# Kernel optimization log

Hardware: AMD Instinct MI355X
Metric: run time of the kernel (lower is better)

The kernel has to match this reference:

```python
import jax, jax.numpy as jnp
import numpy as np

# Constants matching init_kwargs
N_HEADS = 8
D_MODEL = 256
PATCH_NUM = 128
D_K = D_MODEL // N_HEADS  # 32
TEMP = 0.5
EPS = 1e-10


def setup_inputs() -> dict:
    key = jax.random.key(0)
    ks = jax.random.split(key, 20)
    s = 0.02
    d, h, n = D_MODEL, N_HEADS, PATCH_NUM
    inp = {
        "x": jax.random.normal(ks[0], (32, n, d), dtype=jnp.float32),
        "gumbel_u": jax.random.uniform(ks[1], (h, n, n, 2), dtype=jnp.float32),
        "memory_w": jax.random.normal(ks[2], (n, h * d), dtype=jnp.float32) * s,
        "fc_out_w": jax.random.normal(ks[3], (2 * d, d), dtype=jnp.float32) * s,
        "fc_out_b": jnp.zeros((d,), jnp.float32),
        "fc_cat_w": jax.random.normal(ks[4], (d, 2), dtype=jnp.float32) * s,
        "fc_cat_b": jnp.zeros((2,), jnp.float32),
        "wq": jax.random.normal(ks[5], (d, d), dtype=jnp.float32) * s,
        "bq": jnp.zeros((d,), jnp.float32),
        "wk": jax.random.normal(ks[6], (d, d), dtype=jnp.float32) * s,
        "bk": jnp.zeros((d,), jnp.float32),
        "wv": jax.random.normal(ks[7], (d, d), dtype=jnp.float32) * s,
        "bv": jnp.zeros((d,), jnp.float32),
        "out_w": jax.random.normal(ks[8], (d, d), dtype=jnp.float32) * s,
        "out_b": jnp.zeros((d,), jnp.float32),
        "mlp_w1": jax.random.normal(ks[9], (d, d), dtype=jnp.float32) * s,
        "mlp_b1": jnp.zeros((d,), jnp.float32),
        "mlp_w2": jax.random.normal(ks[10], (d, d), dtype=jnp.float32) * s,
        "mlp_b2": jnp.zeros((d,), jnp.float32),
    }
    return inp


def _forward(x, memory_w, fc_out_w, fc_out_b, fc_cat_w, fc_cat_b,
             wq, bq, wk, bk, wv, bv, out_w, out_b,
             mlp_w1, mlp_b1, mlp_w2, mlp_b2, gumbel_u):
    H, N, D = N_HEADS, PATCH_NUM, D_MODEL
    B = x.shape[0]

    # ---- SSConnectionLearning on memory feats ----
    # memory: Embedding(N, d_model*n_heads) -> feats [H, N, D]
    feats = memory_w.reshape(N, H, D).transpose(1, 0, 2)
    # rel_rec gathers row index i (receiver), rel_send gathers col index j (sender)
    senders = jnp.broadcast_to(feats[:, None, :, :], (H, N, N, D))   # feats[j]
    receivers = jnp.broadcast_to(feats[:, :, None, :], (H, N, N, D))  # feats[i]
    pair = jnp.concatenate([senders, receivers], axis=-1)  # [H,N,N,2D]
    hdn = jax.nn.relu(jnp.einsum('hijc,cd->hijd', pair, fc_out_w) + fc_out_b)
    logits = jnp.einsum('hijd,dk->hijk', hdn, fc_cat_w) + fc_cat_b  # [H,N,N,2]

    # gumbel-softmax, hard=True, straight-through
    g = -jnp.log(-jnp.log(gumbel_u + EPS) + EPS)
    y_soft = jax.nn.softmax((logits + g) / TEMP, axis=-1)
    y_hard = jax.nn.one_hot(jnp.argmax(y_soft, axis=-1), 2, dtype=y_soft.dtype)
    y = jax.lax.stop_gradient(y_hard - y_soft) + y_soft
    conn = y[..., 1]  # [H,N,N] learned sparse connection mask

    # ---- PatchIntegration (GELU MLP, dropout = identity in eval) ----
    xm = jax.nn.gelu(x @ mlp_w1 + mlp_b1)
    xm = xm @ mlp_w2 + mlp_b2

    # ---- Multihead attention masked by connection matrix ----
    q = (xm @ wq + bq).reshape(B, N, H, D_K).transpose(0, 2, 1, 3)  # [B,H,N,dk]
    k = (xm @ wk + bk).reshape(B, N, H, D_K).transpose(0, 2, 1, 3)
    v = (xm @ wv + bv).reshape(B, N, H, D_K).transpose(0, 2, 1, 3)
    scale = D_K ** -0.5
    scores = jnp.einsum('bhqd,bhkd->bhqk', q, k) * scale
    # additive mask: blocked where conn==0 (large negative keeps softmax finite)
    scores = scores + (conn[None] - 1.0) * 1e9
    attn = jax.nn.softmax(scores, axis=-1)
    out = jnp.einsum('bhqk,bhkd->bhqd', attn, v)
    out = out.transpose(0, 2, 1, 3).reshape(B, N, H * D_K)
    out = out @ out_w + out_b
    return out


def reference(x, gumbel_u, memory_w, fc_out_w, fc_out_b, fc_cat_w, fc_cat_b,
              wq, bq, wk, bk, wv, bv, out_w, out_b,
              mlp_w1, mlp_b1, mlp_w2, mlp_b2):
    return _forward(x, memory_w, fc_out_w, fc_out_b, fc_cat_w, fc_cat_b,
                    wq, bq, wk, bk, wv, bv, out_w, out_b,
                    mlp_w1, mlp_b1, mlp_w2, mlp_b2, gumbel_u)
```

## Files before the change

kernel.cpp:

```cpp
#include <hip/hip_runtime.h>
#include <hip/hip_bf16.h>
#include <math.h>


typedef short short8 __attribute__((ext_vector_type(8)));
typedef float f32x4 __attribute__((ext_vector_type(4)));

union V8 { uint4 u; short8 s; };

__device__ __forceinline__ float gelu_f(float x) {
    float inner = 0.7978845608028654f * (x + 0.044715f * x * x * x);
    return 0.5f * x * (1.0f + tanhf(inner));
}

__device__ __forceinline__ void split_bf16(float x, ushort& h, ushort& l) {
    __hip_bfloat16 bh = __float2bfloat16(x);
    float hf = __bfloat162float(bh);
    __hip_bfloat16 bl = __float2bfloat16(x - hf);
    h = __builtin_bit_cast(ushort, bh);
    l = __builtin_bit_cast(ushort, bl);
}

__device__ __forceinline__ ushort bf16bits(float x) {
    return __builtin_bit_cast(ushort, __float2bfloat16(x));
}
__device__ __forceinline__ float bits_to_f(ushort v) {
    return __builtin_bit_cast(float, ((uint)v) << 16);
}
__device__ __forceinline__ uint pk(float a, float b) {
    return (uint)bf16bits(a) | ((uint)bf16bits(b) << 16);
}
__device__ __forceinline__ short8 lds_frag(const ushort* p) {
    V8 v; v.u = *(const uint4*)p; return v.s;
}

__global__ __launch_bounds__(256) void k_wprep(
    const float* __restrict__ w0, const float* __restrict__ w1,
    const float* __restrict__ w2, const float* __restrict__ w3,
    const float* __restrict__ w4, const float* __restrict__ w5,
    const float* __restrict__ w6, const float* __restrict__ w7,
    ushort* __restrict__ hi, ushort* __restrict__ lo) {
    int bx = blockIdx.x;
    int m = bx >> 4, ks = (bx >> 1) & 7, nh = bx & 1;
    const float* W = m == 0 ? w0 : m == 1 ? w1 : m == 2 ? w2 : m == 3 ? w3 :
                     m == 4 ? w4 : m == 5 ? w5 : m == 6 ? w6 : w7;
    ushort* Hm = hi + m * 65536;
    ushort* Lm = lo + m * 65536;
    __shared__ __align__(16) float xs[32 * 132];
    int t = threadIdx.x;
    #pragma unroll
    for (int p = 0; p < 4; ++p) {
        int idx = p * 256 + t;
        int row = idx >> 5, c4 = (idx & 31) * 4;
        *(float4*)(xs + row * 132 + c4) =
            *(const float4*)(W + (ks * 32 + row) * 256 + nh * 128 + c4);
    }
    __syncthreads();
    int lane = t & 63, lr = lane & 15, quad = lane >> 4;
    #pragma unroll
    for (int it = 0; it < 2; ++it) {
        int tgl = (t >> 6) + 4 * it;
        int tg = nh * 8 + tgl;
        int nl = tgl * 16 + lr;
        ushort hb[8], lb[8];
        #pragma unroll
        for (int j = 0; j < 8; ++j)
            split_bf16(xs[(quad * 8 + j) * 132 + nl], hb[j], lb[j]);
        uint4 ph = { (uint)hb[0] | ((uint)hb[1] << 16), (uint)hb[2] | ((uint)hb[3] << 16),
                     (uint)hb[4] | ((uint)hb[5] << 16), (uint)hb[6] | ((uint)hb[7] << 16) };
        uint4 pl = { (uint)lb[0] | ((uint)lb[1] << 16), (uint)lb[2] | ((uint)lb[3] << 16),
                     (uint)lb[4] | ((uint)lb[5] << 16), (uint)lb[6] | ((uint)lb[7] << 16) };
        int idx = ((tg * 8 + ks) * 64 + lane) * 8;
        *(uint4*)(Hm + idx) = ph;
        *(uint4*)(Lm + idx) = pl;
    }
}

__global__ __launch_bounds__(256) void k_featproj(
    const float* __restrict__ memory_w,
    const ushort* __restrict__ Whi, const ushort* __restrict__ Wlo,
    float* __restrict__ A, float* __restrict__ Bm) {
    __shared__ __align__(16) ushort xhi[16 * 264], xlo[16 * 264];
    int t = threadIdx.x;
    int rt = blockIdx.x;
    int msel = blockIdx.y & 1, cq = blockIdx.y >> 1;
    #pragma unroll
    for (int ii = 0; ii < 4; ++ii) {
        int f4 = ii * 256 + t;
        int rr = f4 >> 6, c = (f4 & 63) * 4;
        int r = rt * 16 + rr;
        int h = r >> 7, n = r & 127;
        float4 xv = *(const float4*)(memory_w + n * 2048 + h * 256 + c);
        ushort hh[4], ll[4];
        split_bf16(xv.x, hh[0], ll[0]); split_bf16(xv.y, hh[1], ll[1]);
        split_bf16(xv.z, hh[2], ll[2]); split_bf16(xv.w, hh[3], ll[3]);
        uint2 ph = { (uint)hh[0] | ((uint)hh[1] << 16), (uint)hh[2] | ((uint)hh[3] << 16) };
        uint2 pl = { (uint)ll[0] | ((uint)ll[1] << 16), (uint)ll[2] | ((uint)ll[3] << 16) };
        *(uint2*)(xhi + rr * 264 + c) = ph;
        *(uint2*)(xlo + rr * 264 + c) = pl;
    }
    __syncthreads();
    int l = t & 63, w = t >> 6;
    int lr = l & 15, quad = l >> 4;
    int tg = cq * 4 + w;
    const uint4* H4 = (const uint4*)(Whi + (6 + msel) * 65536);
    const uint4* L4 = (const uint4*)(Wlo + (6 + msel) * 65536);
    const ushort* ah = xhi + lr * 264 + quad * 8;
    const ushort* al = xlo + lr * 264 + quad * 8;
    f32x4 acc = {};
    #pragma unroll 4
    for (int ks = 0; ks < 8; ++ks) {
        short8 a_h = lds_frag(ah + ks * 32);
        short8 a_l = lds_frag(al + ks * 32);
        int off = (tg * 8 + ks) * 64 + l;
        V8 bh, bl; bh.u = H4[off]; bl.u = L4[off];
        acc = __builtin_amdgcn_mfma_f32_16x16x32_bf16(a_h, bh.s, acc, 0, 0, 0);
        acc = __builtin_amdgcn_mfma_f32_16x16x32_bf16(a_l, bh.s, acc, 0, 0, 0);
        acc = __builtin_amdgcn_mfma_f32_16x16x32_bf16(a_h, bl.s, acc, 0, 0, 0);
    }
    float* O = msel ? Bm : A;
    int n0 = tg * 16 + lr;
    #pragma unroll
    for (int r = 0; r < 4; ++r)
        O[(rt * 16 + quad * 4 + r) * 256 + n0] = acc[r];
}

__global__ __launch_bounds__(256) void k_conn(
    const float* __restrict__ A, const float* __restrict__ Bm,
    const float* __restrict__ fc_out_b, const float* __restrict__ fc_cat_w,
    const float* __restrict__ fc_cat_b, const float* __restrict__ gumbel_u,
    ushort* __restrict__ maskb) {
    int bx = blockIdx.x;
    int h = bx >> 6, it = (bx >> 3) & 7, jt = bx & 7;
    int i0 = it * 16, j0 = jt * 16;
    int t = threadIdx.x;
    int il = t >> 4, jl = t & 15;
    __shared__ __align__(16) float sA[16 * 260], sB[16 * 260];
    #pragma unroll
    for (int p = 0; p < 4; ++p) {
        int idx = p * 256 + t;
        int rr = idx >> 6, c = (idx & 63) * 4;
        *(float4*)(sA + rr * 260 + c) =
            *(const float4*)(A + (h * 128 + j0 + rr) * 256 + c);
        float4 bv = *(const float4*)(Bm + (h * 128 + i0 + rr) * 256 + c);
        float4 fb = *(const float4*)(fc_out_b + c);
        bv.x += fb.x; bv.y += fb.y; bv.z += fb.z; bv.w += fb.w;
        *(float4*)(sB + rr * 260 + c) = bv;
    }
    __syncthreads();
    const float* Ar = sA + jl * 260;
    const float* Br = sB + il * 260;
    float l0 = fc_cat_b[0], l1 = fc_cat_b[1];
    #pragma unroll 4
    for (int d4 = 0; d4 < 64; ++d4) {
        int d = d4 * 4;
        float4 av = *(const float4*)(Ar + d);
        float4 bv = *(const float4*)(Br + d);
        float4 cwA = *(const float4*)(fc_cat_w + d * 2);
        float4 cwB = *(const float4*)(fc_cat_w + d * 2 + 4);
        float h0 = fmaxf(av.x + bv.x, 0.f);
        float h1 = fmaxf(av.y + bv.y, 0.f);
        float h2 = fmaxf(av.z + bv.z, 0.f);
        float h3 = fmaxf(av.w + bv.w, 0.f);
        l0 += h0 * cwA.x + h1 * cwA.z + h2 * cwB.x + h3 * cwB.z;
        l1 += h0 * cwA.y + h1 * cwA.w + h2 * cwB.y + h3 * cwB.w;
    }
    int i = i0 + il, j = j0 + jl;
    float2 uu = *(const float2*)(gumbel_u + ((h * 128 + i) * 128 + j) * 2);
    float g0 = -logf(-logf(uu.x + 1e-10f) + 1e-10f);
    float g1 = -logf(-logf(uu.y + 1e-10f) + 1e-10f);
    bool on = (l1 + g1) > (l0 + g0);
    maskb[(h * 128 + i) * 128 + j] = bf16bits(on ? 0.f : -1e9f);
}

template <int ACT>
__global__ __launch_bounds__(256) void k_gemm16(
    const float* __restrict__ X, const ushort* __restrict__ Whi,
    const ushort* __restrict__ Wlo, const float* __restrict__ bias,
    float* __restrict__ Y) {
    __shared__ __align__(16) ushort xhi[16 * 264], xlo[16 * 264];
    int t = threadIdx.x;
    int r0 = blockIdx.x * 16;
    #pragma unroll
    for (int ii = 0; ii < 4; ++ii) {
        int f4 = ii * 256 + t;
        int row = f4 >> 6, c = (f4 & 63) * 4;
        float4 xv = *(const float4*)(X + (r0 + row) * 256 + c);
        ushort h[4], l[4];
        split_bf16(xv.x, h[0], l[0]); split_bf16(xv.y, h[1], l[1]);
        split_bf16(xv.z, h[2], l[2]); split_bf16(xv.w, h[3], l[3]);
        uint2 ph = { (uint)h[0] | ((uint)h[1] << 16), (uint)h[2] | ((uint)h[3] << 16) };
        uint2 pl = { (uint)l[0] | ((uint)l[1] << 16), (uint)l[2] | ((uint)l[3] << 16) };
        *(uint2*)(xhi + row * 264 + c) = ph;
        *(uint2*)(xlo + row * 264 + c) = pl;
    }
    __syncthreads();
    int l = t & 63, w = t >> 6;
    int lr = l & 15, quad = l >> 4;
    int tg = blockIdx.y * 4 + w;
    const ushort* ah = xhi + lr * 264 + quad * 8;
    const ushort* al = xlo + lr * 264 + quad * 8;
    const uint4* H4 = (const uint4*)Whi;
    const uint4* L4 = (const uint4*)Wlo;
    f32x4 acc = {};
    #pragma unroll 4
    for (int ks = 0; ks < 8; ++ks) {
        short8 a_h = lds_frag(ah + ks * 32);
        short8 a_l = lds_frag(al + ks * 32);
        int off = (tg * 8 + ks) * 64 + l;
        V8 bh, bl; bh.u = H4[off]; bl.u = L4[off];
        acc = __builtin_amdgcn_mfma_f32_16x16x32_bf16(a_h, bh.s, acc, 0, 0, 0);
        acc = __builtin_amdgcn_mfma_f32_16x16x32_bf16(a_l, bh.s, acc, 0, 0, 0);
        acc = __builtin_amdgcn_mfma_f32_16x16x32_bf16(a_h, bl.s, acc, 0, 0, 0);
    }
    int n0 = tg * 16 + lr;
    float bs = bias[n0];
    #pragma unroll
    for (int r = 0; r < 4; ++r) {
        float o = acc[r] + bs;
        if (ACT) o = gelu_f(o);
        Y[(r0 + quad * 4 + r) * 256 + n0] = o;
    }
}

__global__ __launch_bounds__(256) void k_qkv(
    const float* __restrict__ X, const ushort* __restrict__ Whi,
    const ushort* __restrict__ Wlo,
    const float* __restrict__ Bq, const float* __restrict__ Bk,
    const float* __restrict__ Bv,
    float* __restrict__ Q, float* __restrict__ K, float* __restrict__ V) {
    __shared__ __align__(16) ushort xhi[16 * 264], xlo[16 * 264];
    int t = threadIdx.x;
    int r0 = blockIdx.x * 16;
    int osel = blockIdx.y >> 2, cq = blockIdx.y & 3;
    #pragma unroll
    for (int ii = 0; ii < 4; ++ii) {
        int f4 = ii * 256 + t;
        int row = f4 >> 6, c = (f4 & 63) * 4;
        float4 xv = *(const float4*)(X + (r0 + row) * 256 + c);
        ushort h[4], l[4];
        split_bf16(xv.x, h[0], l[0]); split_bf16(xv.y, h[1], l[1]);
        split_bf16(xv.z, h[2], l[2]); split_bf16(xv.w, h[3], l[3]);
        uint2 ph = { (uint)h[0] | ((uint)h[1] << 16), (uint)h[2] | ((uint)h[3] << 16) };
        uint2 pl = { (uint)l[0] | ((uint)l[1] << 16), (uint)l[2] | ((uint)l[3] << 16) };
        *(uint2*)(xhi + row * 264 + c) = ph;
        *(uint2*)(xlo + row * 264 + c) = pl;
    }
    __syncthreads();
    int l = t & 63, w = t >> 6;
    int lr = l & 15, quad = l >> 4;
    int tg = cq * 4 + w;
    const ushort* ah = xhi + lr * 264 + quad * 8;
    const ushort* al = xlo + lr * 264 + quad * 8;
    const uint4* H4 = (const uint4*)(Whi + (2 + osel) * 65536);
    const uint4* L4 = (const uint4*)(Wlo + (2 + osel) * 65536);
    f32x4 acc = {};
    #pragma unroll 4
    for (int ks = 0; ks < 8; ++ks) {
        short8 a_h = lds_frag(ah + ks * 32);
        short8 a_l = lds_frag(al + ks * 32);
        int off = (tg * 8 + ks) * 64 + l;
        V8 bh, bl; bh.u = H4[off]; bl.u = L4[off];
        acc = __builtin_amdgcn_mfma_f32_16x16x32_bf16(a_h, bh.s, acc, 0, 0, 0);
        acc = __builtin_amdgcn_mfma_f32_16x16x32_bf16(a_l, bh.s, acc, 0, 0, 0);
        acc = __builtin_amdgcn_mfma_f32_16x16x32_bf16(a_h, bl.s, acc, 0, 0, 0);
    }
    const float* Bp = osel == 0 ? Bq : osel == 1 ? Bk : Bv;
    float* O = osel == 0 ? Q : osel == 1 ? K : V;
    int n0 = tg * 16 + lr;
    float bs = Bp[n0];
    #pragma unroll
    for (int r = 0; r < 4; ++r)
        O[(r0 + quad * 4 + r) * 256 + n0] = acc[r] + bs;
}

__global__ __launch_bounds__(256) void k_attn_mfma(
    const float* __restrict__ Q, const float* __restrict__ K,
    const float* __restrict__ V, const ushort* __restrict__ maskb,
    float* __restrict__ AO) {
    int bx = blockIdx.x;
    int b = bx >> 4, h = (bx >> 1) & 7, rh = bx & 1;
    int t = threadIdx.x;
    int lane = t & 63, w = t >> 6;
    __shared__ __align__(16) ushort vT[32 * 136];
    __shared__ __align__(16) ushort ps[64 * 136];
    #pragma unroll
    for (int it = 0; it < 4; ++it) {
        int f4 = it * 256 + t;
        int key = f4 >> 3, dq = (f4 & 7) * 4;
        float4 vv = *(const float4*)(V + b * 32768 + key * 256 + h * 32 + dq);
        vT[(dq + 0) * 136 + key] = bf16bits(vv.x);
        vT[(dq + 1) * 136 + key] = bf16bits(vv.y);
        vT[(dq + 2) * 136 + key] = bf16bits(vv.z);
        vT[(dq + 3) * 136 + key] = bf16bits(vv.w);
    }
    __syncthreads();
    int lr = lane & 15, quad = lane >> 4;
    int rt = rh * 4 + w;
    const float* qp = Q + b * 32768 + (rt * 16 + lr) * 256 + h * 32 + quad * 8;
    float4 q0 = *(const float4*)qp, q1 = *(const float4*)(qp + 4);
    V8 af;
    af.u.x = pk(q0.x, q0.y); af.u.y = pk(q0.z, q0.w);
    af.u.z = pk(q1.x, q1.y); af.u.w = pk(q1.z, q1.w);
    f32x4 s[8];
    #pragma unroll
    for (int ct = 0; ct < 8; ++ct) {
        const float* kp = K + b * 32768 + (ct * 16 + lr) * 256 + h * 32 + quad * 8;
        float4 k0 = *(const float4*)kp, k1 = *(const float4*)(kp + 4);
        V8 bf_;
        bf_.u.x = pk(k0.x, k0.y); bf_.u.y = pk(k0.z, k0.w);
        bf_.u.z = pk(k1.x, k1.y); bf_.u.w = pk(k1.z, k1.w);
        f32x4 z = {0.f, 0.f, 0.f, 0.f};
        s[ct] = __builtin_amdgcn_mfma_f32_16x16x32_bf16(af.s, bf_.s, z, 0, 0, 0);
    }
    const float scale = 0.17677669529663687f;
    const ushort* mrow = maskb + h * 16384;
    #pragma unroll
    for (int r = 0; r < 4; ++r) {
        int lrow = w * 16 + quad * 4 + r;
        int grow = rt * 16 + quad * 4 + r;
        float sv[8];
        float mx = -3.0e38f;
        #pragma unroll
        for (int ct = 0; ct < 8; ++ct) {
            float bias = bits_to_f(mrow[grow * 128 + ct * 16 + lr]);
            sv[ct] = s[ct][r] * scale + bias;
            mx = fmaxf(mx, sv[ct]);
        }
        mx = fmaxf(mx, __shfl_xor(mx, 1));
        mx = fmaxf(mx, __shfl_xor(mx, 2));
        mx = fmaxf(mx, __shfl_xor(mx, 4));
        mx = fmaxf(mx, __shfl_xor(mx, 8));
        float sum = 0.f;
        #pragma unroll
        for (int ct = 0; ct < 8; ++ct) {
            sv[ct] = __expf(sv[ct] - mx);
            sum += sv[ct];
        }
        sum += __shfl_xor(sum, 1);
        sum += __shfl_xor(sum, 2);
        sum += __shfl_xor(sum, 4);
        sum += __shfl_xor(sum, 8);
        float iv = 1.f / sum;
        #pragma unroll
        for (int ct = 0; ct < 8; ++ct)
            ps[lrow * 136 + ct * 16 + lr] = bf16bits(sv[ct] * iv);
    }
    f32x4 o0 = {}, o1 = {};
    #pragma unroll
    for (int kk = 0; kk < 4; ++kk) {
        short8 pa = lds_frag(ps + (w * 16 + lr) * 136 + kk * 32 + quad * 8);
        short8 v0 = lds_frag(vT + lr * 136 + kk * 32 + quad * 8);
        short8 v1 = lds_frag(vT + (16 + lr) * 136 + kk * 32 + quad * 8);
        o0 = __builtin_amdgcn_mfma_f32_16x16x32_bf16(pa, v0, o0, 0, 0, 0);
        o1 = __builtin_amdgcn_mfma_f32_16x16x32_bf16(pa, v1, o1, 0, 0, 0);
    }
    #pragma unroll
    for (int r = 0; r < 4; ++r) {
        int grow = rt * 16 + quad * 4 + r;
        float* op = AO + b * 32768 + grow * 256 + h * 32;
        op[lr] = o0[r];
        op[16 + lr] = o1[r];
    }
}

extern "C" void kernel_launch(void* const* d_in, const int* in_sizes, int n_in,
                              void* d_out, int out_size, void* d_ws, size_t ws_size,
                              hipStream_t stream) {
    const float* x        = (const float*)d_in[0];
    const float* gumbel_u = (const float*)d_in[1];
    const float* memory_w = (const float*)d_in[2];
    const float* fc_out_w = (const float*)d_in[3];
    const float* fc_out_b = (const float*)d_in[4];
    const float* fc_cat_w = (const float*)d_in[5];
    const float* fc_cat_b = (const float*)d_in[6];
    const float* wq       = (const float*)d_in[7];
    const float* bq       = (const float*)d_in[8];
    const float* wk       = (const float*)d_in[9];
    const float* bk       = (const float*)d_in[10];
    const float* wv_      = (const float*)d_in[11];
    const float* bv_      = (const float*)d_in[12];
    const float* out_w    = (const float*)d_in[13];
    const float* out_b    = (const float*)d_in[14];
    const float* mlp_w1   = (const float*)d_in[15];
    const float* mlp_b1   = (const float*)d_in[16];
    const float* mlp_w2   = (const float*)d_in[17];
    const float* mlp_b2   = (const float*)d_in[18];

    float* ws    = (float*)d_ws;
    float* A     = ws;
    float* Bm    = ws + 262144;
    ushort* mask = (ushort*)(ws + 524288);
    float* hbuf  = ws + 589824;
    float* xm    = ws + 1638400;
    float* q     = ws + 2686976;
    float* k     = ws + 3735552;
    float* v     = ws + 4784128;
    float* ao    = ws + 5832704;
    ushort* wf_hi = (ushort*)(ws + 6881280);
    ushort* wf_lo = wf_hi + 8 * 65536;
    float* out   = (float*)d_out;

    k_wprep<<<dim3(128), dim3(256), 0, stream>>>(
        mlp_w1, mlp_w2, wq, wk, wv_, out_w, fc_out_w, fc_out_w + 65536,
        wf_hi, wf_lo);
    k_featproj<<<dim3(64, 8), dim3(256), 0, stream>>>(memory_w, wf_hi, wf_lo, A, Bm);
    k_conn<<<dim3(512), dim3(256), 0, stream>>>(A, Bm, fc_out_b, fc_cat_w, fc_cat_b,
                                                gumbel_u, mask);
    k_gemm16<1><<<dim3(256, 4), dim3(256), 0, stream>>>(x, wf_hi + 0 * 65536,
                                                        wf_lo + 0 * 65536, mlp_b1, hbuf);
    k_gemm16<0><<<dim3(256, 4), dim3(256), 0, stream>>>(hbuf, wf_hi + 1 * 65536,
                                                        wf_lo + 1 * 65536, mlp_b2, xm);
    k_qkv<<<dim3(256, 12), dim3(256), 0, stream>>>(xm, wf_hi, wf_lo, bq, bk, bv_, q, k, v);
    k_attn_mfma<<<dim3(512), dim3(256), 0, stream>>>(q, k, v, mask, ao);
    k_gemm16<0><<<dim3(256, 4), dim3(256), 0, stream>>>(ao, wf_hi + 5 * 65536,
                                                        wf_lo + 5 * 65536, out_b, out);
}
```

Baseline: 161.4 us.

## Fuse all stages into one persistent cooperative kernel with grid syncs

Replaces the eight separate launches with a single cooperative kernel of 512 blocks that runs every stage in sequence, separated by grid-wide barriers. Independent stages (feature projection with MLP1, connection mask with MLP2) now share a phase, and the GEMM phases are reshaped so each block computes two column tiles instead of one. If the cooperative launch fails, it falls back to six per-phase launches. The aim is to remove launch overhead and the gaps between kernels. The cost is grid-sync latency and less parallelism per GEMM phase.

```diff
diff --git a/kernel.cpp b/kernel.cpp
--- a/kernel.cpp
+++ b/kernel.cpp
@@ -1,18 +1,35 @@
 #include <hip/hip_runtime.h>
+#include <hip/hip_cooperative_groups.h>
 #include <hip/hip_bf16.h>
 #include <math.h>
 
+namespace cg = cooperative_groups;
+
 
 typedef short short8 __attribute__((ext_vector_type(8)));
 typedef float f32x4 __attribute__((ext_vector_type(4)));
 
 union V8 { uint4 u; short8 s; };
+
+struct Params {
+    const float *x, *gumbel_u, *memory_w, *fc_out_w, *fc_out_b, *fc_cat_w, *fc_cat_b;
+    const float *wq, *bq, *wk, *bk, *wv, *bv, *out_w, *out_b;
+    const float *mlp_w1, *mlp_b1, *mlp_w2, *mlp_b2;
+    float *A, *Bm, *hbuf, *xm, *q, *k, *v, *ao, *out;
+    ushort *mask, *wf_hi, *wf_lo;
+};
+
+union SMem {
+    struct { ushort xhi[16 * 264]; ushort xlo[16 * 264]; } g;
+    struct { float xs[32 * 132]; } w;
+    struct { float sA[16 * 260]; float sB[16 * 260]; } c;
+    struct { ushort vT[32 * 136]; ushort ps[64 * 136]; } a;
+};
 
 __device__ __forceinline__ float gelu_f(float x) {
     float inner = 0.7978845608028654f * (x + 0.044715f * x * x * x);
     return 0.5f * x * (1.0f + tanhf(inner));
 }
-
 __device__ __forceinline__ void split_bf16(float x, ushort& h, ushort& l) {
     __hip_bfloat16 bh = __float2bfloat16(x);
     float hf = __bfloat162float(bh);
@@ -20,7 +37,6 @@
     h = __builtin_bit_cast(ushort, bh);
     l = __builtin_bit_cast(ushort, bl);
 }
-
 __device__ __forceinline__ ushort bf16bits(float x) {
     return __builtin_bit_cast(ushort, __float2bfloat16(x));
 }
@@ -34,25 +50,19 @@
     V8 v; v.u = *(const uint4*)p; return v.s;
 }
 
-__global__ __launch_bounds__(256) void k_wprep(
-    const float* __restrict__ w0, const float* __restrict__ w1,
-    const float* __restrict__ w2, const float* __restrict__ w3,
-    const float* __restrict__ w4, const float* __restrict__ w5,
-    const float* __restrict__ w6, const float* __restrict__ w7,
-    ushort* __restrict__ hi, ushort* __restrict__ lo) {
-    int bx = blockIdx.x;
-    int m = bx >> 4, ks = (bx >> 1) & 7, nh = bx & 1;
-    const float* W = m == 0 ? w0 : m == 1 ? w1 : m == 2 ? w2 : m == 3 ? w3 :
-                     m == 4 ? w4 : m == 5 ? w5 : m == 6 ? w6 : w7;
-    ushort* Hm = hi + m * 65536;
-    ushort* Lm = lo + m * 65536;
-    __shared__ __align__(16) float xs[32 * 132];
-    int t = threadIdx.x;
+__device__ void ph_wprep(const Params& P, SMem& sm, int bi, int t) {
+    if (bi >= 128) return;
+    int m = bi >> 4, ks = (bi >> 1) & 7, nh = bi & 1;
+    const float* Wm[8] = { P.mlp_w1, P.mlp_w2, P.wq, P.wk, P.wv, P.out_w,
+                           P.fc_out_w, P.fc_out_w + 65536 };
+    const float* W = Wm[m];
+    ushort* Hm = P.wf_hi + m * 65536;
+    ushort* Lm = P.wf_lo + m * 65536;
     #pragma unroll
     for (int p = 0; p < 4; ++p) {
         int idx = p * 256 + t;
         int row = idx >> 5, c4 = (idx & 31) * 4;
-        *(float4*)(xs + row * 132 + c4) =
+        *(float4*)(sm.w.xs + row * 132 + c4) =
             *(const float4*)(W + (ks * 32 + row) * 256 + nh * 128 + c4);
     }
     __syncthreads();
@@ -65,7 +75,7 @@
         ushort hb[8], lb[8];
         #pragma unroll
         for (int j = 0; j < 8; ++j)
-            split_bf16(xs[(quad * 8 + j) * 132 + nl], hb[j], lb[j]);
+            split_bf16(sm.w.xs[(quad * 8 + j) * 132 + nl], hb[j], lb[j]);
         uint4 ph = { (uint)hb[0] | ((uint)hb[1] << 16), (uint)hb[2] | ((uint)hb[3] << 16),
                      (uint)hb[4] | ((uint)hb[5] << 16), (uint)hb[6] | ((uint)hb[7] << 16) };
         uint4 pl = { (uint)lb[0] | ((uint)lb[1] << 16), (uint)lb[2] | ((uint)lb[3] << 16),
@@ -76,111 +86,8 @@
     }
 }
 
-__global__ __launch_bounds__(256) void k_featproj(
-    const float* __restrict__ memory_w,
-    const ushort* __restrict__ Whi, const ushort* __restrict__ Wlo,
-    float* __restrict__ A, float* __restrict__ Bm) {
-    __shared__ __align__(16) ushort xhi[16 * 264], xlo[16 * 264];
-    int t = threadIdx.x;
-    int rt = blockIdx.x;
-    int msel = blockIdx.y & 1, cq = blockIdx.y >> 1;
-    #pragma unroll
-    for (int ii = 0; ii < 4; ++ii) {
-        int f4 = ii * 256 + t;
-        int rr = f4 >> 6, c = (f4 & 63) * 4;
-        int r = rt * 16 + rr;
-        int h = r >> 7, n = r & 127;
-        float4 xv = *(const float4*)(memory_w + n * 2048 + h * 256 + c);
-        ushort hh[4], ll[4];
-        split_bf16(xv.x, hh[0], ll[0]); split_bf16(xv.y, hh[1], ll[1]);
-        split_bf16(xv.z, hh[2], ll[2]); split_bf16(xv.w, hh[3], ll[3]);
-        uint2 ph = { (uint)hh[0] | ((uint)hh[1] << 16), (uint)hh[2] | ((uint)hh[3] << 16) };
-        uint2 pl = { (uint)ll[0] | ((uint)ll[1] << 16), (uint)ll[2] | ((uint)ll[3] << 16) };
-        *(uint2*)(xhi + rr * 264 + c) = ph;
-        *(uint2*)(xlo + rr * 264 + c) = pl;
-    }
-    __syncthreads();
-    int l = t & 63, w = t >> 6;
-    int lr = l & 15, quad = l >> 4;
-    int tg = cq * 4 + w;
-    const uint4* H4 = (const uint4*)(Whi + (6 + msel) * 65536);
-    const uint4* L4 = (const uint4*)(Wlo + (6 + msel) * 65536);
-    const ushort* ah = xhi + lr * 264 + quad * 8;
-    const ushort* al = xlo + lr * 264 + quad * 8;
-    f32x4 acc = {};
-    #pragma unroll 4
-    for (int ks = 0; ks < 8; ++ks) {
-        short8 a_h = lds_frag(ah + ks * 32);
-        short8 a_l = lds_frag(al + ks * 32);
-        int off = (tg * 8 + ks) * 64 + l;
-        V8 bh, bl; bh.u = H4[off]; bl.u = L4[off];
-        acc = __builtin_amdgcn_mfma_f32_16x16x32_bf16(a_h, bh.s, acc, 0, 0, 0);
-        acc = __builtin_amdgcn_mfma_f32_16x16x32_bf16(a_l, bh.s, acc, 0, 0, 0);
-        acc = __builtin_amdgcn_mfma_f32_16x16x32_bf16(a_h, bl.s, acc, 0, 0, 0);
-    }
-    float* O = msel ? Bm : A;
-    int n0 = tg * 16 + lr;
-    #pragma unroll
-    for (int r = 0; r < 4; ++r)
-        O[(rt * 16 + quad * 4 + r) * 256 + n0] = acc[r];
-}
-
-__global__ __launch_bounds__(256) void k_conn(
-    const float* __restrict__ A, const float* __restrict__ Bm,
-    const float* __restrict__ fc_out_b, const float* __restrict__ fc_cat_w,
-    const float* __restrict__ fc_cat_b, const float* __restrict__ gumbel_u,
-    ushort* __restrict__ maskb) {
-    int bx = blockIdx.x;
-    int h = bx >> 6, it = (bx >> 3) & 7, jt = bx & 7;
-    int i0 = it * 16, j0 = jt * 16;
-    int t = threadIdx.x;
-    int il = t >> 4, jl = t & 15;
-    __shared__ __align__(16) float sA[16 * 260], sB[16 * 260];
-    #pragma unroll
-    for (int p = 0; p < 4; ++p) {
-        int idx = p * 256 + t;
-        int rr = idx >> 6, c = (idx & 63) * 4;
-        *(float4*)(sA + rr * 260 + c) =
-            *(const float4*)(A + (h * 128 + j0 + rr) * 256 + c);
-        float4 bv = *(const float4*)(Bm + (h * 128 + i0 + rr) * 256 + c);
-        float4 fb = *(const float4*)(fc_out_b + c);
-        bv.x += fb.x; bv.y += fb.y; bv.z += fb.z; bv.w += fb.w;
-        *(float4*)(sB + rr * 260 + c) = bv;
-    }
-    __syncthreads();
-    const float* Ar = sA + jl * 260;
-    const float* Br = sB + il * 260;
-    float l0 = fc_cat_b[0], l1 = fc_cat_b[1];
-    #pragma unroll 4
-    for (int d4 = 0; d4 < 64; ++d4) {
-        int d = d4 * 4;
-        float4 av = *(const float4*)(Ar + d);
-        float4 bv = *(const float4*)(Br + d);
-        float4 cwA = *(const float4*)(fc_cat_w + d * 2);
-        float4 cwB = *(const float4*)(fc_cat_w + d * 2 + 4);
-        float h0 = fmaxf(av.x + bv.x, 0.f);
-        float h1 = fmaxf(av.y + bv.y, 0.f);
-        float h2 = fmaxf(av.z + bv.z, 0.f);
-        float h3 = fmaxf(av.w + bv.w, 0.f);
-        l0 += h0 * cwA.x + h1 * cwA.z + h2 * cwB.x + h3 * cwB.z;
-        l1 += h0 * cwA.y + h1 * cwA.w + h2 * cwB.y + h3 * cwB.w;
-    }
-    int i = i0 + il, j = j0 + jl;
-    float2 uu = *(const float2*)(gumbel_u + ((h * 128 + i) * 128 + j) * 2);
-    float g0 = -logf(-logf(uu.x + 1e-10f) + 1e-10f);
-    float g1 = -logf(-logf(uu.y + 1e-10f) + 1e-10f);
-    bool on = (l1 + g1) > (l0 + g0);
-    maskb[(h * 128 + i) * 128 + j] = bf16bits(on ? 0.f : -1e9f);
-}
-
-template <int ACT>
-__global__ __launch_bounds__(256) void k_gemm16(
-    const float* __restrict__ X, const ushort* __restrict__ Whi,
-    const ushort* __restrict__ Wlo, const float* __restrict__ bias,
-    float* __restrict__ Y) {
-    __shared__ __align__(16) ushort xhi[16 * 264], xlo[16 * 264];
-    int t = threadIdx.x;
-    int r0 = blockIdx.x * 16;
+__device__ void stage_x(SMem& sm, const float* X, int r0, int t) {
+    __syncthreads();
     #pragma unroll
     for (int ii = 0; ii < 4; ++ii) {
         int f4 = ii * 256 + t;
@@ -191,15 +98,17 @@
         split_bf16(xv.z, h[2], l[2]); split_bf16(xv.w, h[3], l[3]);
         uint2 ph = { (uint)h[0] | ((uint)h[1] << 16), (uint)h[2] | ((uint)h[3] << 16) };
         uint2 pl = { (uint)l[0] | ((uint)l[1] << 16), (uint)l[2] | ((uint)l[3] << 16) };
-        *(uint2*)(xhi + row * 264 + c) = ph;
-        *(uint2*)(xlo + row * 264 + c) = pl;
-    }
-    __syncthreads();
-    int l = t & 63, w = t >> 6;
-    int lr = l & 15, quad = l >> 4;
-    int tg = blockIdx.y * 4 + w;
-    const ushort* ah = xhi + lr * 264 + quad * 8;
-    const ushort* al = xlo + lr * 264 + quad * 8;
+        *(uint2*)(sm.g.xhi + row * 264 + c) = ph;
+        *(uint2*)(sm.g.xlo + row * 264 + c) = pl;
+    }
+    __syncthreads();
+}
+
+__device__ f32x4 gemm_wave(const SMem& sm, const ushort* Whi, const ushort* Wlo,
+                           int tg, int lane) {
+    int lr = lane & 15, quad = lane >> 4;
+    const ushort* ah = sm.g.xhi + lr * 264 + quad * 8;
+    const ushort* al = sm.g.xlo + lr * 264 + quad * 8;
     const uint4* H4 = (const uint4*)Whi;
     const uint4* L4 = (const uint4*)Wlo;
     f32x4 acc = {};
@@ -207,97 +116,164 @@
     for (int ks = 0; ks < 8; ++ks) {
         short8 a_h = lds_frag(ah + ks * 32);
         short8 a_l = lds_frag(al + ks * 32);
-        int off = (tg * 8 + ks) * 64 + l;
+        int off = (tg * 8 + ks) * 64 + lane;
         V8 bh, bl; bh.u = H4[off]; bl.u = L4[off];
         acc = __builtin_amdgcn_mfma_f32_16x16x32_bf16(a_h, bh.s, acc, 0, 0, 0);
         acc = __builtin_amdgcn_mfma_f32_16x16x32_bf16(a_l, bh.s, acc, 0, 0, 0);
         acc = __builtin_amdgcn_mfma_f32_16x16x32_bf16(a_h, bl.s, acc, 0, 0, 0);
     }
-    int n0 = tg * 16 + lr;
-    float bs = bias[n0];
-    #pragma unroll
-    for (int r = 0; r < 4; ++r) {
-        float o = acc[r] + bs;
-        if (ACT) o = gelu_f(o);
-        Y[(r0 + quad * 4 + r) * 256 + n0] = o;
-    }
-}
-
-__global__ __launch_bounds__(256) void k_qkv(
-    const float* __restrict__ X, const ushort* __restrict__ Whi,
-    const ushort* __restrict__ Wlo,
-    const float* __restrict__ Bq, const float* __restrict__ Bk,
-    const float* __restrict__ Bv,
-    float* __restrict__ Q, float* __restrict__ K, float* __restrict__ V) {
-    __shared__ __align__(16) ushort xhi[16 * 264], xlo[16 * 264];
-    int t = threadIdx.x;
-    int r0 = blockIdx.x * 16;
-    int osel = blockIdx.y >> 2, cq = blockIdx.y & 3;
+    return acc;
+}
+
+__device__ void ph_featproj(const Params& P, SMem& sm, int bi, int t) {
+    int rt = bi & 63;
+    int y = bi >> 6;
+    int msel = y & 1, cq = y >> 1;
+    __syncthreads();
     #pragma unroll
     for (int ii = 0; ii < 4; ++ii) {
         int f4 = ii * 256 + t;
-        int row = f4 >> 6, c = (f4 & 63) * 4;
-        float4 xv = *(const float4*)(X + (r0 + row) * 256 + c);
-        ushort h[4], l[4];
-        split_bf16(xv.x, h[0], l[0]); split_bf16(xv.y, h[1], l[1]);
-        split_bf16(xv.z, h[2], l[2]); split_bf16(xv.w, h[3], l[3]);
-        uint2 ph = { (uint)h[0] | ((uint)h[1] << 16), (uint)h[2] | ((uint)h[3] << 16) };
-        uint2 pl = { (uint)l[0] | ((uint)l[1] << 16), (uint)l[2] | ((uint)l[3] << 16) };
-        *(uint2*)(xhi + row * 264 + c) = ph;
-        *(uint2*)(xlo + row * 264 + c) = pl;
-    }
-    __syncthreads();
-    int l = t & 63, w = t >> 6;
-    int lr = l & 15, quad = l >> 4;
+        int rr = f4 >> 6, c = (f4 & 63) * 4;
+        int r = rt * 16 + rr;
+        int h = r >> 7, n = r & 127;
+        float4 xv = *(const float4*)(P.memory_w + n * 2048 + h * 256 + c);
+        ushort hh[4], ll[4];
+        split_bf16(xv.x, hh[0], ll[0]); split_bf16(xv.y, hh[1], ll[1]);
+        split_bf16(xv.z, hh[2], ll[2]); split_bf16(xv.w, hh[3], ll[3]);
+        uint2 ph = { (uint)hh[0] | ((uint)hh[1] << 16), (uint)hh[2] | ((uint)hh[3] << 16) };
+        uint2 pl = { (uint)ll[0] | ((uint)ll[1] << 16), (uint)ll[2] | ((uint)ll[3] << 16) };
+        *(uint2*)(sm.g.xhi + rr * 264 + c) = ph;
+        *(uint2*)(sm.g.xlo + rr * 264 + c) = pl;
+    }
+    __syncthreads();
+    int lane = t & 63, w = t >> 6;
+    int lr = lane & 15, quad = lane >> 4;
     int tg = cq * 4 + w;
-    const ushort* ah = xhi + lr * 264 + quad * 8;
-    const ushort* al = xlo + lr * 264 + quad * 8;
-    const uint4* H4 = (const uint4*)(Whi + (2 + osel) * 65536);
-    const uint4* L4 = (const uint4*)(Wlo + (2 + osel) * 65536);
-    f32x4 acc = {};
+    f32x4 acc = gemm_wave(sm, P.wf_hi + (6 + msel) * 65536,
+                          P.wf_lo + (6 + msel) * 65536, tg, lane);
+    float* O = msel ? P.Bm : P.A;
+    int n0 = tg * 16 + lr;
+    #pragma unroll
+    for (int r = 0; r < 4; ++r)
+        O[(rt * 16 + quad * 4 + r) * 256 + n0] = acc[r];
+}
+
+__device__ void ph_mlp1(const Params& P, SMem& sm, int bi, int t) {
+    int rt = bi & 255, h2 = bi >> 8;
+    stage_x(sm, P.x, rt * 16, t);
+    int lane = t & 63, w = t >> 6;
+    int lr = lane & 15, quad = lane >> 4;
+    #pragma unroll
+    for (int i = 0; i < 2; ++i) {
+        int tg = (h2 * 2 + i) * 4 + w;
+        f32x4 acc = gemm_wave(sm, P.wf_hi, P.wf_lo, tg, lane);
+        int n0 = tg * 16 + lr;
+        float bs = P.mlp_b1[n0];
+        #pragma unroll
+        for (int r = 0; r < 4; ++r)
+            P.hbuf[(rt * 16 + quad * 4 + r) * 256 + n0] = gelu_f(acc[r] + bs);
+    }
+}
+
+__device__ void ph_conn(const Params& P, SMem& sm, int bi, int t) {
+    int h = bi >> 6, it = (bi >> 3) & 7, jt = bi & 7;
+    int i0 = it * 16, j0 = jt * 16;
+    int il = t >> 4, jl = t & 15;
+    __syncthreads();
+    #pragma unroll
+    for (int p = 0; p < 4; ++p) {
+        int idx = p * 256 + t;
+        int rr = idx >> 6, c = (idx & 63) * 4;
+        *(float4*)(sm.c.sA + rr * 260 + c) =
+            *(const float4*)(P.A + (h * 128 + j0 + rr) * 256 + c);
+        float4 bv = *(const float4*)(P.Bm + (h * 128 + i0 + rr) * 256 + c);
+        float4 fb = *(const float4*)(P.fc_out_b + c);
+        bv.x += fb.x; bv.y += fb.y; bv.z += fb.z; bv.w += fb.w;
+        *(float4*)(sm.c.sB + rr * 260 + c) = bv;
+    }
+    __syncthreads();
+    const float* Ar = sm.c.sA + jl * 260;
+    const float* Br = sm.c.sB + il * 260;
+    float l0 = P.fc_cat_b[0], l1 = P.fc_cat_b[1];
     #pragma unroll 4
-    for (int ks = 0; ks < 8; ++ks) {
-        short8 a_h = lds_frag(ah + ks * 32);
-        short8 a_l = lds_frag(al + ks * 32);
-        int off = (tg * 8 + ks) * 64 + l;
-        V8 bh, bl; bh.u = H4[off]; bl.u = L4[off];
-        acc = __builtin_amdgcn_mfma_f32_16x16x32_bf16(a_h, bh.s, acc, 0, 0, 0);
-        acc = __builtin_amdgcn_mfma_f32_16x16x32_bf16(a_l, bh.s, acc, 0, 0, 0);
-        acc = __builtin_amdgcn_mfma_f32_16x16x32_bf16(a_h, bl.s, acc, 0, 0, 0);
-    }
-    const float* Bp = osel == 0 ? Bq : osel == 1 ? Bk : Bv;
-    float* O = osel == 0 ? Q : osel == 1 ? K : V;
-    int n0 = tg * 16 + lr;
-    float bs = Bp[n0];
-    #pragma unroll
-    for (int r = 0; r < 4; ++r)
-        O[(r0 + quad * 4 + r) * 256 + n0] = acc[r] + bs;
-}
-
-__global__ __launch_bounds__(256) void k_attn_mfma(
-    const float* __restrict__ Q, const float* __restrict__ K,
-    const float* __restrict__ V, const ushort* __restrict__ maskb,
-    float* __restrict__ AO) {
-    int bx = blockIdx.x;
-    int b = bx >> 4, h = (bx >> 1) & 7, rh = bx & 1;
-    int t = threadIdx.x;
-    int lane = t & 63, w = t >> 6;
-    __shared__ __align__(16) ushort vT[32 * 136];
-    __shared__ __align__(16) ushort ps[64 * 136];
+    for (int d4 = 0; d4 < 64; ++d4) {
+        int d = d4 * 4;
+        float4 av = *(const float4*)(Ar + d);
+        float4 bv = *(const float4*)(Br + d);
+        float4 cwA = *(const float4*)(P.fc_cat_w + d * 2);
+        float4 cwB = *(const float4*)(P.fc_cat_w + d * 2 + 4);
+        float h0 = fmaxf(av.x + bv.x, 0.f);
+        float h1 = fmaxf(av.y + bv.y, 0.f);
+        float h2 = fmaxf(av.z + bv.z, 0.f);
+        float h3 = fmaxf(av.w + bv.w, 0.f);
+        l0 += h0 * cwA.x + h1 * cwA.z + h2 * cwB.x + h3 * cwB.z;
+        l1 += h0 * cwA.y + h1 * cwA.w + h2 * cwB.y + h3 * cwB.w;
+    }
+    int i = i0 + il, j = j0 + jl;
+    float2 uu = *(const float2*)(P.gumbel_u + ((h * 128 + i) * 128 + j) * 2);
+    float g0 = -logf(-logf(uu.x + 1e-10f) + 1e-10f);
+    float g1 = -logf(-logf(uu.y + 1e-10f) + 1e-10f);
+    bool on = (l1 + g1) > (l0 + g0);
+    P.mask[(h * 128 + i) * 128 + j] = bf16bits(on ? 0.f : -1e9f);
+}
+
+__device__ void ph_mlp2(const Params& P, SMem& sm, int bi, int t) {
+    int rt = bi & 255, h2 = bi >> 8;
+    stage_x(sm, P.hbuf, rt * 16, t);
+    int lane = t & 63, w = t >> 6;
+    int lr = lane & 15, quad = lane >> 4;
+    #pragma unroll
+    for (int i = 0; i < 2; ++i) {
+        int tg = (h2 * 2 + i) * 4 + w;
+        f32x4 acc = gemm_wave(sm, P.wf_hi + 65536, P.wf_lo + 65536, tg, lane);
+        int n0 = tg * 16 + lr;
+        float bs = P.mlp_b2[n0];
+        #pragma unroll
+        for (int r = 0; r < 4; ++r)
+            P.xm[(rt * 16 + quad * 4 + r) * 256 + n0] = acc[r] + bs;
+    }
+}
+
+__device__ void ph_qkv(const Params& P, SMem& sm, int bi, int t) {
+    int rt = bi & 255, h2 = bi >> 8;
+    stage_x(sm, P.xm, rt * 16, t);
+    int lane = t & 63, w = t >> 6;
+    int lr = lane & 15, quad = lane >> 4;
+    #pragma unroll
+    for (int j = 0; j < 6; ++j) {
+        int c = h2 * 6 + j;
+        int osel = c >> 2, cq = c & 3;
+        int tg = cq * 4 + w;
+        f32x4 acc = gemm_wave(sm, P.wf_hi + (2 + osel) * 65536,
+                              P.wf_lo + (2 + osel) * 65536, tg, lane);
+        const float* Bp = osel == 0 ? P.bq : osel == 1 ? P.bk : P.bv;
+        float* O = osel == 0 ? P.q : osel == 1 ? P.k : P.v;
+        int n0 = tg * 16 + lr;
+        float bs = Bp[n0];
+        #pragma unroll
+        for (int r = 0; r < 4; ++r)
+            O[(rt * 16 + quad * 4 + r) * 256 + n0] = acc[r] + bs;
+    }
+}
+
+__device__ void ph_attn(const Params& P, SMem& sm, int bi, int t) {
+    int b = bi >> 4, h = (bi >> 1) & 7, rh = bi & 1;
+    int lane = t & 63, w = t >> 6;
+    __syncthreads();
     #pragma unroll
     for (int it = 0; it < 4; ++it) {
         int f4 = it * 256 + t;
         int key = f4 >> 3, dq = (f4 & 7) * 4;
-        float4 vv = *(const float4*)(V + b * 32768 + key * 256 + h * 32 + dq);
-        vT[(dq + 0) * 136 + key] = bf16bits(vv.x);
-        vT[(dq + 1) * 136 + key] = bf16bits(vv.y);
-        vT[(dq + 2) * 136 + key] = bf16bits(vv.z);
-        vT[(dq + 3) * 136 + key] = bf16bits(vv.w);
+        float4 vv = *(const float4*)(P.v + b * 32768 + key * 256 + h * 32 + dq);
+        sm.a.vT[(dq + 0) * 136 + key] = bf16bits(vv.x);
+        sm.a.vT[(dq + 1) * 136 + key] = bf16bits(vv.y);
+        sm.a.vT[(dq + 2) * 136 + key] = bf16bits(vv.z);
+        sm.a.vT[(dq + 3) * 136 + key] = bf16bits(vv.w);
     }
     __syncthreads();
     int lr = lane & 15, quad = lane >> 4;
     int rt = rh * 4 + w;
-    const float* qp = Q + b * 32768 + (rt * 16 + lr) * 256 + h * 32 + quad * 8;
+    const float* qp = P.q + b * 32768 + (rt * 16 + lr) * 256 + h * 32 + quad * 8;
     float4 q0 = *(const float4*)qp, q1 = *(const float4*)(qp + 4);
     V8 af;
     af.u.x = pk(q0.x, q0.y); af.u.y = pk(q0.z, q0.w);
@@ -305,7 +281,7 @@
     f32x4 s[8];
     #pragma unroll
     for (int ct = 0; ct < 8; ++ct) {
-        const float* kp = K + b * 32768 + (ct * 16 + lr) * 256 + h * 32 + quad * 8;
+        const float* kp = P.k + b * 32768 + (ct * 16 + lr) * 256 + h * 32 + quad * 8;
         float4 k0 = *(const float4*)kp, k1 = *(const float4*)(kp + 4);
         V8 bf_;
         bf_.u.x = pk(k0.x, k0.y); bf_.u.y = pk(k0.z, k0.w);
@@ -314,7 +290,7 @@
         s[ct] = __builtin_amdgcn_mfma_f32_16x16x32_bf16(af.s, bf_.s, z, 0, 0, 0);
     }
     const float scale = 0.17677669529663687f;
-    const ushort* mrow = maskb + h * 16384;
+    const ushort* mrow = P.mask + h * 16384;
     #pragma unroll
     for (int r = 0; r < 4; ++r) {
         int lrow = w * 16 + quad * 4 + r;
@@ -344,75 +320,121 @@
         float iv = 1.f / sum;
         #pragma unroll
         for (int ct = 0; ct < 8; ++ct)
-            ps[lrow * 136 + ct * 16 + lr] = bf16bits(sv[ct] * iv);
+            sm.a.ps[lrow * 136 + ct * 16 + lr] = bf16bits(sv[ct] * iv);
     }
     f32x4 o0 = {}, o1 = {};
     #pragma unroll
     for (int kk = 0; kk < 4; ++kk) {
-        short8 pa = lds_frag(ps + (w * 16 + lr) * 136 + kk * 32 + quad * 8);
-        short8 v0 = lds_frag(vT + lr * 136 + kk * 32 + quad * 8);
-        short8 v1 = lds_frag(vT + (16 + lr) * 136 + kk * 32 + quad * 8);
+        short8 pa = lds_frag(sm.a.ps + (w * 16 + lr) * 136 + kk * 32 + quad * 8);
+        short8 v0 = lds_frag(sm.a.vT + lr * 136 + kk * 32 + quad * 8);
+        short8 v1 = lds_frag(sm.a.vT + (16 + lr) * 136 + kk * 32 + quad * 8);
         o0 = __builtin_amdgcn_mfma_f32_16x16x32_bf16(pa, v0, o0, 0, 0, 0);
         o1 = __builtin_amdgcn_mfma_f32_16x16x32_bf16(pa, v1, o1, 0, 0, 0);
     }
     #pragma unroll
     for (int r = 0; r < 4; ++r) {
         int grow = rt * 16 + quad * 4 + r;
-        float* op = AO + b * 32768 + grow * 256 + h * 32;
+        float* op = P.ao + b * 32768 + grow * 256 + h * 32;
         op[lr] = o0[r];
         op[16 + lr] = o1[r];
     }
+}
+
+__device__ void ph_out(const Params& P, SMem& sm, int bi, int t) {
+    int rt = bi & 255, h2 = bi >> 8;
+    stage_x(sm, P.ao, rt * 16, t);
+    int lane = t & 63, w = t >> 6;
+    int lr = lane & 15, quad = lane >> 4;
+    #pragma unroll
+    for (int i = 0; i < 2; ++i) {
+        int tg = (h2 * 2 + i) * 4 + w;
+        f32x4 acc = gemm_wave(sm, P.wf_hi + 5 * 65536, P.wf_lo + 5 * 65536, tg, lane);
+        int n0 = tg * 16 + lr;
+        float bs = P.out_b[n0];
+        #pragma unroll
+        for (int r = 0; r < 4; ++r)
+            P.out[(rt * 16 + quad * 4 + r) * 256 + n0] = acc[r] + bs;
+    }
+}
+
+__global__ __launch_bounds__(256, 2) void k_mega(Params P) {
+    cg::grid_group grid = cg::this_grid();
+    __shared__ SMem sm;
+    int bi = blockIdx.x, t = threadIdx.x;
+    ph_wprep(P, sm, bi, t);
+    grid.sync();
+    ph_featproj(P, sm, bi, t);
+    ph_mlp1(P, sm, bi, t);
+    grid.sync();
+    ph_conn(P, sm, bi, t);
+    ph_mlp2(P, sm, bi, t);
+    grid.sync();
+    ph_qkv(P, sm, bi, t);
+    grid.sync();
+    ph_attn(P, sm, bi, t);
+    grid.sync();
+    ph_out(P, sm, bi, t);
+}
+
+template <int PH>
+__global__ __launch_bounds__(256, 2) void k_phase(Params P) {
+    __shared__ SMem sm;
+    int bi = blockIdx.x, t = threadIdx.x;
+    if (PH == 0) ph_wprep(P, sm, bi, t);
+    if (PH == 1) { ph_featproj(P, sm, bi, t); ph_mlp1(P, sm, bi, t); }
+    if (PH == 2) { ph_conn(P, sm, bi, t); ph_mlp2(P, sm, bi, t); }
+    if (PH == 3) ph_qkv(P, sm, bi, t);
+    if (PH == 4) ph_attn(P, sm, bi, t);
+    if (PH == 5) ph_out(P, sm, bi, t);
 }
 
 extern "C" void kernel_launch(void* const* d_in, const int* in_sizes, int n_in,
                               void* d_out, int out_size, void* d_ws, size_t ws_size,
                               hipStream_t stream) {
-    const float* x        = (const float*)d_in[0];
-    const float* gumbel_u = (const float*)d_in[1];
-    const float* memory_w = (const float*)d_in[2];
-    const float* fc_out_w = (const float*)d_in[3];
-    const float* fc_out_b = (const float*)d_in[4];
-    const float* fc_cat_w = (const float*)d_in[5];
-    const float* fc_cat_b = (const float*)d_in[6];
-    const float* wq       = (const float*)d_in[7];
-    const float* bq       = (const float*)d_in[8];
-    const float* wk       = (const float*)d_in[9];
-    const float* bk       = (const float*)d_in[10];
-    const float* wv_      = (const float*)d_in[11];
-    const float* bv_      = (const float*)d_in[12];
-    const float* out_w    = (const float*)d_in[13];
-    const float* out_b    = (const float*)d_in[14];
-    const float* mlp_w1   = (const float*)d_in[15];
-    const float* mlp_b1   = (const float*)d_in[16];
-    const float* mlp_w2   = (const float*)d_in[17];
-    const float* mlp_b2   = (const float*)d_in[18];
-
-    float* ws    = (float*)d_ws;
-    float* A     = ws;
-    float* Bm    = ws + 262144;
-    ushort* mask = (ushort*)(ws + 524288);
-    float* hbuf  = ws + 589824;
-    float* xm    = ws + 1638400;
-    float* q     = ws + 2686976;
-    float* k     = ws + 3735552;
-    float* v     = ws + 4784128;
-    float* ao    = ws + 5832704;
-    ushort* wf_hi = (ushort*)(ws + 6881280);
-    ushort* wf_lo = wf_hi + 8 * 65536;
-    float* out   = (float*)d_out;
-
-    k_wprep<<<dim3(128), dim3(256), 0, stream>>>(
-        mlp_w1, mlp_w2, wq, wk, wv_, out_w, fc_out_w, fc_out_w + 65536,
-        wf_hi, wf_lo);
-    k_featproj<<<dim3(64, 8), dim3(256), 0, stream>>>(memory_w, wf_hi, wf_lo, A, Bm);
-    k_conn<<<dim3(512), dim3(256), 0, stream>>>(A, Bm, fc_out_b, fc_cat_w, fc_cat_b,
-                                                gumbel_u, mask);
-    k_gemm16<1><<<dim3(256, 4), dim3(256), 0, stream>>>(x, wf_hi + 0 * 65536,
-                                                        wf_lo + 0 * 65536, mlp_b1, hbuf);
-    k_gemm16<0><<<dim3(256, 4), dim3(256), 0, stream>>>(hbuf, wf_hi + 1 * 65536,
-                                                        wf_lo + 1 * 65536, mlp_b2, xm);
-    k_qkv<<<dim3(256, 12), dim3(256), 0, stream>>>(xm, wf_hi, wf_lo, bq, bk, bv_, q, k, v);
-    k_attn_mfma<<<dim3(512), dim3(256), 0, stream>>>(q, k, v, mask, ao);
-    k_gemm16<0><<<dim3(256, 4), dim3(256), 0, stream>>>(ao, wf_hi + 5 * 65536,
-                                                        wf_lo + 5 * 65536, out_b, out);
-}
+    float* ws = (float*)d_ws;
+    Params P;
+    P.x        = (const float*)d_in[0];
+    P.gumbel_u = (const float*)d_in[1];
+    P.memory_w = (const float*)d_in[2];
+    P.fc_out_w = (const float*)d_in[3];
+    P.fc_out_b = (const float*)d_in[4];
+    P.fc_cat_w = (const float*)d_in[5];
+    P.fc_cat_b = (const float*)d_in[6];
+    P.wq       = (const float*)d_in[7];
+    P.bq       = (const float*)d_in[8];
+    P.wk       = (const float*)d_in[9];
+    P.bk       = (const float*)d_in[10];
+    P.wv       = (const float*)d_in[11];
+    P.bv       = (const float*)d_in[12];
+    P.out_w    = (const float*)d_in[13];
+    P.out_b    = (const float*)d_in[14];
+    P.mlp_w1   = (const float*)d_in[15];
+    P.mlp_b1   = (const float*)d_in[16];
+    P.mlp_w2   = (const float*)d_in[17];
+    P.mlp_b2   = (const float*)d_in[18];
+    P.A     = ws;
+    P.Bm    = ws + 262144;
+    P.mask  = (ushort*)(ws + 524288);
+    P.hbuf  = ws + 589824;
+    P.xm    = ws + 1638400;
+    P.q     = ws + 2686976;
+    P.k     = ws + 3735552;
+    P.v     = ws + 4784128;
+    P.ao    = ws + 5832704;
+    P.wf_hi = (ushort*)(ws + 6881280);
+    P.wf_lo = P.wf_hi + 8 * 65536;
+    P.out   = (float*)d_out;
+
+    void* args[] = { &P };
+    hipError_t e = hipLaunchCooperativeKernel((const void*)k_mega, dim3(512),
+                                              dim3(256), args, 0, stream);
+    if (e != hipSuccess) {
+        (void)hipGetLastError();
+        k_phase<0><<<dim3(512), dim3(256), 0, stream>>>(P);
+        k_phase<1><<<dim3(512), dim3(256), 0, stream>>>(P);
+        k_phase<2><<<dim3(512), dim3(256), 0, stream>>>(P);
+        k_phase<3><<<dim3(512), dim3(256), 0, stream>>>(P);
+        k_phase<4><<<dim3(512), dim3(256), 0, stream>>>(P);
+        k_phase<5><<<dim3(512), dim3(256), 0, stream>>>(P);
+    }
+}
```

Result: slower. 486.5 us (+201.4%).
